# Kernel tuning notes

Hardware: AMD Instinct MI355X
Metric: run time of the kernel (lower is better)

Reference implementation:

```python
import jax, jax.numpy as jnp
import numpy as np

GRID_SIZE = 300


def setup_inputs() -> dict:
    key = jax.random.key(0)
    k1, k2 = jax.random.split(key)
    N, input_dim, out_dim = 2048, 256, 256
    x = jax.random.normal(k1, (N, input_dim), dtype=jnp.float32)
    scale = 1.0 / (np.sqrt(input_dim) * np.sqrt(GRID_SIZE))
    coeffs = jax.random.normal(k2, (2, out_dim, input_dim, GRID_SIZE), dtype=jnp.float32) * scale
    bias = jnp.zeros((1, out_dim), dtype=jnp.float32)
    return {"x": x, "coeffs": coeffs, "bias": bias}


def reference(x, coeffs, bias):
    # x: [N, I]; coeffs: [2, J, I, K]; bias: [1, J]
    grid_size = coeffs.shape[-1]
    k = jnp.arange(1, grid_size + 1, dtype=x.dtype)            # [K]
    ang = x[:, :, None] * k                                    # [N, I, K]
    c = jnp.cos(ang)
    s = jnp.sin(ang)
    # einsum('dbik,djik->bj') with d=2 split into cos/sin parts
    y = jnp.einsum('bik,jik->bj', c, coeffs[0]) + jnp.einsum('bik,jik->bj', s, coeffs[1])
    y = y + bias
    return y
```

## Files before the change

### kernel.cpp

```cpp
#include <hip/hip_runtime.h>
#include <stdint.h>

#define NB 2048
#define NI 256
#define NJ 256
#define GK 300
#define KPAD 320
#define KK_PER_I (2*KPAD)
#define NKC2 (NI*KK_PER_I/16)
#define CH32_PER_I 20
#define SPLITK 32
#define II_PER_S (NI / SPLITK)
#define BM 128

typedef __bf16 bf16x8 __attribute__((ext_vector_type(8)));
typedef __bf16 bf16x2 __attribute__((ext_vector_type(2)));
typedef float  f32x16 __attribute__((ext_vector_type(16)));

__device__ __forceinline__ void sincos2pi(float ang, float& c, float& s) {
  float r = ang * 0.15915494309189535f;
  r = r - floorf(r);
  c = __builtin_amdgcn_cosf(r);
  s = __builtin_amdgcn_sinf(r);
}

__device__ __forceinline__ unsigned int pkbf(float c, float s) {
  bf16x2 p; p.x = (__bf16)c; p.y = (__bf16)s;
  return __builtin_bit_cast(unsigned int, p);
}

__device__ __forceinline__ void rot(float& c, float& s, float cr, float sr) {
  float nc = c * cr - s * sr;
  s = s * cr + c * sr;
  c = nc;
}

__global__ __launch_bounds__(256) void convert_b(const float* __restrict__ coeffs,
                                                 uint4* __restrict__ bw4) {
  const int bid = blockIdx.x;
  const int i  = bid >> 3;
  const int jt = bid & 7;
  const int t  = (int)threadIdx.x;
  const int n2 = t & 31;
  const int gl = t >> 5;
  const int j  = jt * 32 + n2;

  const float4* r0 = (const float4*)(coeffs + (size_t)(j * NI + i) * GK);
  const float4* r1 = (const float4*)(coeffs + (size_t)((NJ + j) * NI + i) * GK);

  #pragma unroll
  for (int p = 0; p < 10; p++) {
    const int g = p * 8 + gl;
    uint4 w = {0u, 0u, 0u, 0u};
    if (g < GK / 4) {
      float4 a = r0[g];
      float4 b = r1[g];
      w.x = pkbf(a.x, b.x);
      w.y = pkbf(a.y, b.y);
      w.z = pkbf(a.z, b.z);
      w.w = pkbf(a.w, b.w);
    }
    const int kc2 = i * 40 + (g >> 1);
    bw4[(size_t)(kc2 * 8 + jt) * 64 + n2 + 32 * (g & 1)] = w;
  }
}

__global__ __launch_bounds__(256) void init_out(const float* __restrict__ bias,
                                                float* __restrict__ out) {
  const int tid = blockIdx.x * 256 + threadIdx.x;
  float4 b = ((const float4*)bias)[tid & 63];
  ((float4*)out)[tid] = b;
}

__global__ __launch_bounds__(256, 2) void fkan_gemm(const float* __restrict__ x,
                                                    const uint4* __restrict__ bw4,
                                                    float* __restrict__ out) {
  const int bid = blockIdx.x;
  const int mt = bid & 15;
  const int s  = bid >> 4;
  const int m0 = mt * BM;

  const int t    = (int)threadIdx.x;
  const int lane = t & 63;
  const int wave = t >> 6;
  const int wr = wave >> 1;
  const int wc = wave & 1;
  const int q2 = lane >> 5;
  const int ln = lane & 31;

  f32x16 acc[2][4];
  #pragma unroll
  for (int mm = 0; mm < 2; mm++)
    #pragma unroll
    for (int nn = 0; nn < 4; nn++)
      #pragma unroll
      for (int r = 0; r < 16; r++)
        acc[mm][nn][r] = 0.f;

  const uint4* bp = bw4 + (size_t)(wc * 4) * 64 + lane;

  int kc2 = s * (NKC2 / SPLITK);
  uint4 bcur[8], bnxt[8];
  #pragma unroll
  for (int q = 0; q < 8; q++)
    bcur[q] = bp[(size_t)(kc2 + (q >> 2)) * 512 + (q & 3) * 64];

  float stc[2], sts[2], c1a[2], s1a[2], c5a[2], s5a[2];

  #pragma unroll 1
  for (int ii = 0; ii < II_PER_S; ii++) {
    const int i = s * II_PER_S + ii;
    #pragma unroll
    for (int mm = 0; mm < 2; mm++) {
      const float xv = x[(m0 + wr * 64 + mm * 32 + ln) * NI + i];
      sincos2pi(xv, c1a[mm], s1a[mm]);
      sincos2pi(5.f * xv, c5a[mm], s5a[mm]);
      sincos2pi(xv * (float)(q2 * 4 + 1), stc[mm], sts[mm]);
    }

    #pragma unroll 2
    for (int c = 0; c < CH32_PER_I; c++) {
      const int kc2n = (kc2 + 2 <= NKC2 - 2) ? kc2 + 2 : kc2;
      #pragma unroll
      for (int q = 0; q < 8; q++)
        bnxt[q] = bp[(size_t)(kc2n + (q >> 2)) * 512 + (q & 3) * 64];

      bf16x8 af[2][2];
      #pragma unroll
      for (int mm = 0; mm < 2; mm++) {
        float cc = stc[mm], ss = sts[mm];
        uint4 u0, u1;
        u0.x = pkbf(cc, ss);
        rot(cc, ss, c1a[mm], s1a[mm]); u0.y = pkbf(cc, ss);
        rot(cc, ss, c1a[mm], s1a[mm]); u0.z = pkbf(cc, ss);
        rot(cc, ss, c1a[mm], s1a[mm]); u0.w = pkbf(cc, ss);
        rot(cc, ss, c5a[mm], s5a[mm]);
        u1.x = pkbf(cc, ss);
        rot(cc, ss, c1a[mm], s1a[mm]); u1.y = pkbf(cc, ss);
        rot(cc, ss, c1a[mm], s1a[mm]); u1.z = pkbf(cc, ss);
        rot(cc, ss, c1a[mm], s1a[mm]); u1.w = pkbf(cc, ss);
        rot(cc, ss, c5a[mm], s5a[mm]);
        stc[mm] = cc; sts[mm] = ss;
        af[mm][0] = __builtin_bit_cast(bf16x8, u0);
        af[mm][1] = __builtin_bit_cast(bf16x8, u1);
      }

      #pragma unroll
      for (int ks = 0; ks < 2; ks++)
        #pragma unroll
        for (int nn = 0; nn < 4; nn++) {
          const bf16x8 bfr = __builtin_bit_cast(bf16x8, bcur[ks * 4 + nn]);
          #pragma unroll
          for (int mm = 0; mm < 2; mm++)
            acc[mm][nn] = __builtin_amdgcn_mfma_f32_32x32x16_bf16(
                af[mm][ks], bfr, acc[mm][nn], 0, 0, 0);
        }

      #pragma unroll
      for (int q = 0; q < 8; q++) bcur[q] = bnxt[q];
      kc2 += 2;
    }
  }

  const int cb = wc * 128 + ln;
  #pragma unroll
  for (int mm = 0; mm < 2; mm++)
    #pragma unroll
    for (int nn = 0; nn < 4; nn++)
      #pragma unroll
      for (int r = 0; r < 16; r++) {
        const int row = m0 + wr * 64 + mm * 32 + (r & 3) + 8 * (r >> 2) + 4 * q2;
        atomicAdd(&out[row * NJ + cb + nn * 32], acc[mm][nn][r]);
      }
}

extern "C" void kernel_launch(void* const* d_in, const int* in_sizes, int n_in,
                              void* d_out, int out_size, void* d_ws, size_t ws_size,
                              hipStream_t stream) {
  const float* x      = (const float*)d_in[0];
  const float* coeffs = (const float*)d_in[1];
  const float* bias   = (const float*)d_in[2];
  float* out = (float*)d_out;
  uint4* bw4 = (uint4*)d_ws;

  convert_b<<<dim3(NI * 8), dim3(256), 0, stream>>>(coeffs, bw4);
  init_out<<<dim3(NB * NJ / 4 / 256), dim3(256), 0, stream>>>(bias, out);
  fkan_gemm<<<dim3(16 * SPLITK), dim3(256), 0, stream>>>(x, (const uint4*)bw4, out);
}
```

Before: 448.0 us.

## Split GEMM over N tiles, shrink accumulators, raise occupancy, double-buffer B and x

Each block now covers half of the output columns (128 instead of 256), so the grid doubles across an N-tile index and split-K drops to 24 with uneven i ranges. Per-wave accumulators shrink from 2x4 to 2x2 MFMA tiles, which allows three blocks per CU instead of two. The B-fragment prefetch becomes a ping-pong buffer without register copies, and the next x value is prefetched. The cost is that each block recomputes the sin/cos A fragments for its own N half, so trig and rotation work doubles.

```diff
diff --git a/kernel.cpp b/kernel.cpp
--- a/kernel.cpp
+++ b/kernel.cpp
@@ -9,8 +9,7 @@
 #define KK_PER_I (2*KPAD)
 #define NKC2 (NI*KK_PER_I/16)
 #define CH32_PER_I 20
-#define SPLITK 32
-#define II_PER_S (NI / SPLITK)
+#define SPLITK 24
 #define BM 128
 
 typedef __bf16 bf16x8 __attribute__((ext_vector_type(8)));
@@ -72,12 +71,14 @@
   ((float4*)out)[tid] = b;
 }
 
-__global__ __launch_bounds__(256, 2) void fkan_gemm(const float* __restrict__ x,
+__global__ __launch_bounds__(256, 3) void fkan_gemm(const float* __restrict__ x,
                                                     const uint4* __restrict__ bw4,
                                                     float* __restrict__ out) {
   const int bid = blockIdx.x;
   const int mt = bid & 15;
-  const int s  = bid >> 4;
+  const int r2 = bid >> 4;
+  const int nt = r2 & 1;
+  const int s  = r2 >> 1;
   const int m0 = mt * BM;
 
   const int t    = (int)threadIdx.x;
@@ -88,42 +89,51 @@
   const int q2 = lane >> 5;
   const int ln = lane & 31;
 
-  f32x16 acc[2][4];
+  const int i0 = (s * 256) / SPLITK;
+  const int i1 = ((s + 1) * 256) / SPLITK;
+
+  f32x16 acc[2][2];
   #pragma unroll
   for (int mm = 0; mm < 2; mm++)
     #pragma unroll
-    for (int nn = 0; nn < 4; nn++)
+    for (int nn = 0; nn < 2; nn++)
       #pragma unroll
       for (int r = 0; r < 16; r++)
         acc[mm][nn][r] = 0.f;
 
-  const uint4* bp = bw4 + (size_t)(wc * 4) * 64 + lane;
-
-  int kc2 = s * (NKC2 / SPLITK);
-  uint4 bcur[8], bnxt[8];
-  #pragma unroll
-  for (int q = 0; q < 8; q++)
-    bcur[q] = bp[(size_t)(kc2 + (q >> 2)) * 512 + (q & 3) * 64];
+  const uint4* bp = bw4 + (size_t)(nt * 4 + wc * 2) * 64 + lane;
+
+  int kc2 = i0 * 40;
+  uint4 bufA[4], bufB[4];
+  #pragma unroll
+  for (int f = 0; f < 4; f++)
+    bufA[f] = bp[(size_t)((kc2 + (f >> 1)) * 8 + (f & 1)) * 64];
+
+  const float* xr0 = x + (m0 + wr * 64 + ln) * NI;
+  const float* xr1 = x + (m0 + wr * 64 + 32 + ln) * NI;
+  float xv0 = xr0[i0], xv1 = xr1[i0];
 
   float stc[2], sts[2], c1a[2], s1a[2], c5a[2], s5a[2];
 
   #pragma unroll 1
-  for (int ii = 0; ii < II_PER_S; ii++) {
-    const int i = s * II_PER_S + ii;
-    #pragma unroll
-    for (int mm = 0; mm < 2; mm++) {
-      const float xv = x[(m0 + wr * 64 + mm * 32 + ln) * NI + i];
-      sincos2pi(xv, c1a[mm], s1a[mm]);
-      sincos2pi(5.f * xv, c5a[mm], s5a[mm]);
-      sincos2pi(xv * (float)(q2 * 4 + 1), stc[mm], sts[mm]);
+  for (int ii = i0; ii < i1; ii++) {
+    {
+      const float xv[2] = {xv0, xv1};
+      #pragma unroll
+      for (int mm = 0; mm < 2; mm++) {
+        sincos2pi(xv[mm], c1a[mm], s1a[mm]);
+        sincos2pi(5.f * xv[mm], c5a[mm], s5a[mm]);
+        sincos2pi(xv[mm] * (float)(q2 * 4 + 1), stc[mm], sts[mm]);
+      }
     }
-
-    #pragma unroll 2
-    for (int c = 0; c < CH32_PER_I; c++) {
-      const int kc2n = (kc2 + 2 <= NKC2 - 2) ? kc2 + 2 : kc2;
-      #pragma unroll
-      for (int q = 0; q < 8; q++)
-        bnxt[q] = bp[(size_t)(kc2n + (q >> 2)) * 512 + (q & 3) * 64];
+    const int inx = (ii + 1 < i1) ? ii + 1 : ii;
+    const float xn0 = xr0[inx], xn1 = xr1[inx];
+
+    auto body = [&](uint4* use, uint4* pre) {
+      const int kcp = (kc2 + 2 <= NKC2 - 2) ? kc2 + 2 : kc2;
+      #pragma unroll
+      for (int f = 0; f < 4; f++)
+        pre[f] = bp[(size_t)((kcp + (f >> 1)) * 8 + (f & 1)) * 64];
 
       bf16x8 af[2][2];
       #pragma unroll
@@ -148,25 +158,30 @@
       #pragma unroll
       for (int ks = 0; ks < 2; ks++)
         #pragma unroll
-        for (int nn = 0; nn < 4; nn++) {
-          const bf16x8 bfr = __builtin_bit_cast(bf16x8, bcur[ks * 4 + nn]);
+        for (int nn = 0; nn < 2; nn++) {
+          const bf16x8 bfr = __builtin_bit_cast(bf16x8, use[ks * 2 + nn]);
           #pragma unroll
           for (int mm = 0; mm < 2; mm++)
             acc[mm][nn] = __builtin_amdgcn_mfma_f32_32x32x16_bf16(
                 af[mm][ks], bfr, acc[mm][nn], 0, 0, 0);
         }
-
-      #pragma unroll
-      for (int q = 0; q < 8; q++) bcur[q] = bnxt[q];
       kc2 += 2;
+    };
+
+    #pragma unroll 1
+    for (int cc = 0; cc < CH32_PER_I / 2; cc++) {
+      body(bufA, bufB);
+      body(bufB, bufA);
     }
+
+    xv0 = xn0; xv1 = xn1;
   }
 
-  const int cb = wc * 128 + ln;
+  const int cb = nt * 128 + wc * 64 + ln;
   #pragma unroll
   for (int mm = 0; mm < 2; mm++)
     #pragma unroll
-    for (int nn = 0; nn < 4; nn++)
+    for (int nn = 0; nn < 2; nn++)
       #pragma unroll
       for (int r = 0; r < 16; r++) {
         const int row = m0 + wr * 64 + mm * 32 + (r & 3) + 8 * (r >> 2) + 4 * q2;
@@ -185,5 +200,5 @@
 
   convert_b<<<dim3(NI * 8), dim3(256), 0, stream>>>(coeffs, bw4);
   init_out<<<dim3(NB * NJ / 4 / 256), dim3(256), 0, stream>>>(bias, out);
-  fkan_gemm<<<dim3(16 * SPLITK), dim3(256), 0, stream>>>(x, (const uint4*)bw4, out);
-}
+  fkan_gemm<<<dim3(16 * 2 * SPLITK), dim3(256), 0, stream>>>(x, (const uint4*)bw4, out);
+}
```

Result: no change. 456.4 us (+1.9%).
